# Kernel optimization log

Hardware: AMD Instinct MI355X
Metric: run time of the kernel (lower is better)

The kernel has to match this reference:

```python
import jax, jax.numpy as jnp
import numpy as np

D_MODEL, D_FF, N_EXPERTS, TOP_K = 1024, 2048, 8, 2
B, S = 2, 2048

def setup_inputs() -> dict:
    key = jax.random.key(0)
    k1, k2, k3, k4 = jax.random.split(key, 4)
    scale = 0.02
    return {
        "x": jax.random.normal(k1, (B, S, D_MODEL), dtype=jnp.float32),
        "gate_w": jax.random.normal(k2, (D_MODEL, N_EXPERTS), dtype=jnp.float32) * scale,
        "w1": jax.random.normal(k3, (N_EXPERTS, D_MODEL, D_FF), dtype=jnp.float32) * scale,
        "w2": jax.random.normal(k4, (N_EXPERTS, D_FF, D_MODEL), dtype=jnp.float32) * scale,
    }

def reference(x, gate_w, w1, w2):
    # --- Router (eval mode: no exploration noise, no dropout) ---
    router_logits = jnp.einsum('bsd,de->bse', x, gate_w)          # [B,S,E]
    top_logits, top_idx = jax.lax.top_k(router_logits, TOP_K)      # [B,S,K]
    top_w = jax.nn.softmax(top_logits, axis=-1)                    # [B,S,K]
    # topk indices are distinct per token, so per-(token,expert) combine weight
    # is the sum over k of weight_k * 1[idx_k == e] (matches torch gather/argmax logic)
    combine = jnp.sum(
        jax.nn.one_hot(top_idx, N_EXPERTS, dtype=x.dtype) * top_w[..., None],
        axis=-2)                                                   # [B,S,E]
    # --- Experts: dense-compute formulation of the gather/MLP/scatter loop ---
    h = jax.nn.silu(jnp.einsum('bsd,edf->ebsf', x, w1))            # [E,B,S,Dff]
    y = jnp.einsum('ebsf,efd->ebsd', h, w2)                        # [E,B,S,D]
    out = jnp.einsum('ebsd,bse->bsd', y, combine)                  # [B,S,D]
    return out
```

## Files before the change

### kernel.cpp

```cpp
#include <hip/hip_runtime.h>
#include <cstdint>
#include <cstddef>

#define D_MODEL 1024
#define D_FF    2048
#define N_EXP   8
#define NTOK    4096
#define NASSIGN (NTOK * 2)
#define MAXTILE 72

typedef __bf16 bf16_t;
typedef bf16_t bf16x8 __attribute__((ext_vector_type(8)));
typedef float  f32x4  __attribute__((ext_vector_type(4)));

typedef __attribute__((address_space(3))) void       lds_void;
typedef const __attribute__((address_space(1))) void gl_void;

__device__ __forceinline__ unsigned short f2b(float f) {
  union { float f; unsigned u; } v; v.f = f;
  unsigned u = v.u;
  unsigned r = (u + 0x7FFFu + ((u >> 16) & 1u)) >> 16;
  return (unsigned short)r;
}
__device__ __forceinline__ float b2f(unsigned short b) {
  union { unsigned u; float f; } v; v.u = ((unsigned)b) << 16; return v.f;
}

__device__ __forceinline__ void transpose_tile(
    const float* __restrict__ ein, unsigned short* __restrict__ eout,
    int R, int C, int bx, int by, float (*T)[65], int tid)
{
  const int c0 = bx * 64, r0 = by * 64;
  const int g = tid >> 4;
  const int m = tid & 15;
  #pragma unroll
  for (int i = 0; i < 4; ++i) {
    int r = i * 16 + g;
    float4 v = *(const float4*)(ein + (size_t)(r0 + r) * C + c0 + m * 4);
    T[r][m * 4 + 0] = v.x; T[r][m * 4 + 1] = v.y;
    T[r][m * 4 + 2] = v.z; T[r][m * 4 + 3] = v.w;
  }
  __syncthreads();
  #pragma unroll
  for (int i = 0; i < 4; ++i) {
    int c = i * 16 + g;
    ushort4 o;
    o.x = f2b(T[m * 4 + 0][c]); o.y = f2b(T[m * 4 + 1][c]);
    o.z = f2b(T[m * 4 + 2][c]); o.w = f2b(T[m * 4 + 3][c]);
    *(ushort4*)(eout + (size_t)(c0 + c) * R + r0 + m * 4) = o;
  }
}

__global__ __launch_bounds__(256) void prep_k(
    const float* __restrict__ x, const float* __restrict__ gw,
    const float* __restrict__ w1, const float* __restrict__ w2,
    unsigned short* __restrict__ w1t, unsigned short* __restrict__ w2t,
    int* __restrict__ eidx, float* __restrict__ ewt)
{
  __shared__ float T[64][65];
  const int bid = blockIdx.x;
  const int tid = threadIdx.x;

  if (bid < 4096) {
    int bx = bid & 31, by = (bid >> 5) & 15, e = bid >> 9;
    transpose_tile(w1 + (size_t)e * D_MODEL * D_FF,
                   w1t + (size_t)e * D_MODEL * D_FF,
                   D_MODEL, D_FF, bx, by, T, tid);
    return;
  }
  if (bid < 8192) {
    int b = bid - 4096;
    int bx = b & 15, by = (b >> 4) & 31, e = b >> 9;
    transpose_tile(w2 + (size_t)e * D_MODEL * D_FF,
                   w2t + (size_t)e * D_MODEL * D_FF,
                   D_FF, D_MODEL, bx, by, T, tid);
    return;
  }
  const int rb = bid - 8192;
  const int wv = tid >> 6, lane = tid & 63;
  const int token = rb * 4 + wv;
  const float4* xr4 = (const float4*)(x + (size_t)token * D_MODEL);
  const float4* gw4 = (const float4*)gw;

  float acc[8] = {};
  #pragma unroll
  for (int it = 0; it < 4; ++it) {
    float4 xv = xr4[it * 64 + lane];
    int d0 = it * 256 + lane * 4;
    #pragma unroll
    for (int i = 0; i < 4; ++i) {
      int d = d0 + i;
      float4 g0 = gw4[d * 2];
      float4 g1 = gw4[d * 2 + 1];
      float xs = (i == 0) ? xv.x : (i == 1) ? xv.y : (i == 2) ? xv.z : xv.w;
      acc[0] += xs * g0.x; acc[1] += xs * g0.y;
      acc[2] += xs * g0.z; acc[3] += xs * g0.w;
      acc[4] += xs * g1.x; acc[5] += xs * g1.y;
      acc[6] += xs * g1.z; acc[7] += xs * g1.w;
    }
  }
  #pragma unroll
  for (int m = 1; m < 64; m <<= 1) {
    #pragma unroll
    for (int k = 0; k < 8; ++k) acc[k] += __shfl_xor(acc[k], m);
  }
  if (lane == 0) {
    int i1 = 0; float v1 = acc[0];
    #pragma unroll
    for (int k = 1; k < 8; ++k) if (acc[k] > v1) { v1 = acc[k]; i1 = k; }
    int i2 = -1; float v2 = -1e30f;
    #pragma unroll
    for (int k = 0; k < 8; ++k) if (k != i1 && acc[k] > v2) { v2 = acc[k]; i2 = k; }
    float t  = __expf(v2 - v1);
    float wa = 1.f / (1.f + t);
    float wb = t * wa;
    eidx[token * 2 + 0] = i1; eidx[token * 2 + 1] = i2;
    ewt [token * 2 + 0] = wa; ewt [token * 2 + 1] = wb;
  }
}

__global__ __launch_bounds__(256) void scan_k(
    const int* __restrict__ eidx, const float* __restrict__ ewt,
    int* __restrict__ counts, int* __restrict__ offsets,
    int* __restrict__ rowtok, float* __restrict__ rowwt, int* __restrict__ rowof,
    int* __restrict__ tile_e, int* __restrict__ tile_m0, int* __restrict__ tile_n)
{
  __shared__ int hist[256][9];
  __shared__ int soff[8];
  const int t = threadIdx.x;

  int local[8] = {};
  #pragma unroll 4
  for (int i = 0; i < 32; ++i) local[eidx[t * 32 + i]]++;
  #pragma unroll
  for (int e = 0; e < 8; ++e) hist[t][e] = local[e];
  __syncthreads();

  for (int ofs = 1; ofs < 256; ofs <<= 1) {
    int v[8];
    if (t >= ofs) {
      #pragma unroll
      for (int e = 0; e < 8; ++e) v[e] = hist[t - ofs][e];
    }
    __syncthreads();
    if (t >= ofs) {
      #pragma unroll
      for (int e = 0; e < 8; ++e) hist[t][e] += v[e];
    }
    __syncthreads();
  }

  if (t == 0) {
    int o = 0, tt = 0;
    for (int e = 0; e < 8; ++e) {
      int c = hist[255][e];
      counts[e] = c;
      offsets[e] = o;
      soff[e] = o;
      int nt = (c + 127) >> 7;
      for (int i = 0; i < nt; ++i) { tile_e[tt] = e; tile_m0[tt] = i * 128; ++tt; }
      o += c;
    }
    tile_n[0] = tt;
  }
  __syncthreads();

  int run[8];
  #pragma unroll
  for (int e = 0; e < 8; ++e) run[e] = soff[e] + hist[t][e] - local[e];

  #pragma unroll 4
  for (int i = 0; i < 32; ++i) {
    int b = t * 32 + i;
    int e = eidx[b];
    int row = run[e]++;
    rowtok[row] = b >> 1;
    rowwt[row]  = ewt[b];
    rowof[b]    = row;
  }
}

__global__ __launch_bounds__(256) void gather_k(
    const float* __restrict__ x, const int* __restrict__ rowtok,
    unsigned short* __restrict__ Xe)
{
  const int row = blockIdx.x;
  const int token = rowtok[row];
  const float4* xr = (const float4*)(x + (size_t)token * D_MODEL);
  ushort4* dst = (ushort4*)(Xe + (size_t)row * D_MODEL);
  float4 v = xr[threadIdx.x];
  ushort4 o;
  o.x = f2b(v.x); o.y = f2b(v.y); o.z = f2b(v.z); o.w = f2b(v.w);
  dst[threadIdx.x] = o;
}

template<int K, int N, int NT_LOG2, int MODE>
__global__ __launch_bounds__(256) void moe_gemm_k(
    const unsigned short* __restrict__ A,
    const unsigned short* __restrict__ Bt,
    unsigned short* __restrict__ Hout,
    const int* __restrict__ counts, const int* __restrict__ offsets,
    const float* __restrict__ rowwt,
    const int* __restrict__ tile_e, const int* __restrict__ tile_m0,
    const int* __restrict__ tile_n)
{
  const int t = blockIdx.x >> NT_LOG2;
  if (t >= tile_n[0]) return;
  const int e   = tile_e[t];
  const int m0  = tile_m0[t];
  const int n0  = (blockIdx.x & ((1 << NT_LOG2) - 1)) * 128;
  const int cnt = counts[e];
  const int base = offsets[e];

  __shared__ unsigned short lA[128 * 32];
  __shared__ unsigned short lB[128 * 32];

  const int tid = threadIdx.x;
  const int lane = tid & 63;
  const int wv = tid >> 6;
  const int wm = wv & 1, wn = wv >> 1;
  const int col = lane & 15, quad = lane >> 4;

  const unsigned short* Aseg = A + (size_t)base * K;
  const unsigned short* Bseg = Bt + (size_t)e * ((size_t)N * K);

  const int lrow = lane >> 2;
  const int gch  = (lane & 3) ^ ((lane >> 2) & 3) ^ ((lane >> 4) & 3);

  const int fsw = (col & 3) ^ ((col >> 2) & 3);

  f32x4 acc[4][4] = {};

  for (int k0 = 0; k0 < K; k0 += 32) {
    __syncthreads();
    #pragma unroll
    for (int r = 0; r < 2; ++r) {
      int s = r * 4 + wv;
      int row = s * 16 + lrow;
      const char* gA = (const char*)Aseg + ((size_t)(m0 + row) * K + k0) * 2 + gch * 16;
      const char* gB = (const char*)Bseg + ((size_t)(n0 + row) * K + k0) * 2 + gch * 16;
      __builtin_amdgcn_global_load_lds((gl_void*)gA, (lds_void*)((char*)lA + s * 1024), 16, 0, 0);
      __builtin_amdgcn_global_load_lds((gl_void*)gB, (lds_void*)((char*)lB + s * 1024), 16, 0, 0);
    }
    __syncthreads();

    bf16x8 af[4], bfr[4];
    #pragma unroll
    for (int i = 0; i < 4; ++i) {
      int r = wm * 64 + i * 16 + col;
      int p = quad ^ fsw;
      af[i] = *(const bf16x8*)(lA + r * 32 + p * 8);
    }
    #pragma unroll
    for (int j = 0; j < 4; ++j) {
      int r = wn * 64 + j * 16 + col;
      int p = quad ^ fsw;
      bfr[j] = *(const bf16x8*)(lB + r * 32 + p * 8);
    }
    #pragma unroll
    for (int i = 0; i < 4; ++i)
      #pragma unroll
      for (int j = 0; j < 4; ++j)
        acc[i][j] = __builtin_amdgcn_mfma_f32_16x16x32_bf16(af[i], bfr[j], acc[i][j], 0, 0, 0);
  }

  #pragma unroll
  for (int i = 0; i < 4; ++i) {
    #pragma unroll
    for (int reg = 0; reg < 4; ++reg) {
      int r = m0 + wm * 64 + i * 16 + quad * 4 + reg;
      if (r < cnt) {
        unsigned short* hrow = Hout + (size_t)(base + r) * N + (n0 + wn * 64 + col);
        if (MODE == 1) {
          #pragma unroll
          for (int j = 0; j < 4; ++j) {
            float v = acc[i][j][reg];
            float s = v / (1.f + __expf(-v));
            hrow[j * 16] = f2b(s);
          }
        } else {
          float wgt = rowwt[base + r];
          #pragma unroll
          for (int j = 0; j < 4; ++j)
            hrow[j * 16] = f2b(wgt * acc[i][j][reg]);
        }
      }
    }
  }
}

__global__ __launch_bounds__(256) void combine_k(
    const unsigned short* __restrict__ Y, const int* __restrict__ rowof,
    float* __restrict__ out)
{
  const int token = blockIdx.x;
  const int r1 = rowof[token * 2];
  const int r2 = rowof[token * 2 + 1];
  const int d4 = threadIdx.x;
  ushort4 a = *(const ushort4*)(Y + (size_t)r1 * D_MODEL + d4 * 4);
  ushort4 b = *(const ushort4*)(Y + (size_t)r2 * D_MODEL + d4 * 4);
  float4 o;
  o.x = b2f(a.x) + b2f(b.x);
  o.y = b2f(a.y) + b2f(b.y);
  o.z = b2f(a.z) + b2f(b.z);
  o.w = b2f(a.w) + b2f(b.w);
  *(float4*)(out + (size_t)token * D_MODEL + d4 * 4) = o;
}

extern "C" void kernel_launch(void* const* d_in, const int* in_sizes, int n_in,
                              void* d_out, int out_size, void* d_ws, size_t ws_size,
                              hipStream_t stream) {
  const float* x  = (const float*)d_in[0];
  const float* gw = (const float*)d_in[1];
  const float* w1 = (const float*)d_in[2];
  const float* w2 = (const float*)d_in[3];
  float* out = (float*)d_out;

  char* ws = (char*)d_ws;
  size_t off = 0;
  auto alloc = [&](size_t bytes) -> char* {
    char* p = ws + off; off += (bytes + 255) & ~(size_t)255; return p;
  };
  int*   ctrl    = (int*)alloc(1024);
  int*   counts  = ctrl;
  int*   offsets = ctrl + 8;
  int*   tile_n  = ctrl + 16;
  int*   tile_e  = ctrl + 32;
  int*   tile_m0 = ctrl + 32 + MAXTILE;
  int*   eidx    = (int*)  alloc((size_t)NASSIGN * 4);
  float* ewt     = (float*)alloc((size_t)NASSIGN * 4);
  int*   rowtok  = (int*)  alloc((size_t)NASSIGN * 4);
  float* rowwt   = (float*)alloc((size_t)NASSIGN * 4);
  int*   rowof   = (int*)  alloc((size_t)NASSIGN * 4);
  unsigned short* Xe  = (unsigned short*)alloc((size_t)(NASSIGN + 128) * D_MODEL * 2);
  unsigned short* H   = (unsigned short*)alloc((size_t)(NASSIGN + 128) * D_FF * 2);
  unsigned short* Y   = (unsigned short*)alloc((size_t)(NASSIGN + 128) * D_MODEL * 2);
  unsigned short* w1t = (unsigned short*)alloc((size_t)N_EXP * D_MODEL * D_FF * 2);
  unsigned short* w2t = (unsigned short*)alloc((size_t)N_EXP * D_MODEL * D_FF * 2);

  prep_k<<<8192 + NTOK / 4, 256, 0, stream>>>(x, gw, w1, w2, w1t, w2t, eidx, ewt);
  scan_k<<<1, 256, 0, stream>>>(eidx, ewt, counts, offsets, rowtok, rowwt, rowof,
                                tile_e, tile_m0, tile_n);
  gather_k<<<NASSIGN, 256, 0, stream>>>(x, rowtok, Xe);

  moe_gemm_k<D_MODEL, D_FF, 4, 1><<<MAXTILE * 16, 256, 0, stream>>>(
      Xe, w1t, H, counts, offsets, rowwt, tile_e, tile_m0, tile_n);
  moe_gemm_k<D_FF, D_MODEL, 3, 2><<<MAXTILE * 8, 256, 0, stream>>>(
      H, w2t, Y, counts, offsets, rowwt, tile_e, tile_m0, tile_n);
  combine_k<<<NTOK, 256, 0, stream>>>(Y, rowof, out);
}
```

Before: 355.3 us.

## Transpose weight tile pairs via packed bf16 LDS, warp-shuffle scan, gemm occupancy hint

The weight transpose now does two 64x64 tiles per block. It converts to bf16 before staging, packs pairs into 32-bit LDS words, and issues all global loads up front, halving the block count and LDS traffic. The single-block scan uses 1024 threads with wave-level shuffle prefix sums in place of a shared-memory Hillis-Steele scan with many barriers. The expert GEMMs also gain a min-blocks launch-bounds hint, which may force register spilling.

```diff
diff --git a/kernel.cpp b/kernel.cpp
--- a/kernel.cpp
+++ b/kernel.cpp
@@ -26,28 +26,56 @@
   union { unsigned u; float f; } v; v.u = ((unsigned)b) << 16; return v.f;
 }
 
-__device__ __forceinline__ void transpose_tile(
+__device__ __forceinline__ void transpose_pair(
     const float* __restrict__ ein, unsigned short* __restrict__ eout,
-    int R, int C, int bx, int by, float (*T)[65], int tid)
-{
-  const int c0 = bx * 64, r0 = by * 64;
+    int R, int C, int c00, int r0, unsigned* T0, unsigned* T1, int tid)
+{
   const int g = tid >> 4;
   const int m = tid & 15;
-  #pragma unroll
-  for (int i = 0; i < 4; ++i) {
-    int r = i * 16 + g;
-    float4 v = *(const float4*)(ein + (size_t)(r0 + r) * C + c0 + m * 4);
-    T[r][m * 4 + 0] = v.x; T[r][m * 4 + 1] = v.y;
-    T[r][m * 4 + 2] = v.z; T[r][m * 4 + 3] = v.w;
-  }
-  __syncthreads();
+  const int sh = (g & 1) * 16;
+
+  float4 v[2][4];
+  #pragma unroll
+  for (int t = 0; t < 2; ++t)
+    #pragma unroll
+    for (int i = 0; i < 4; ++i)
+      v[t][i] = *(const float4*)(ein + (size_t)(r0 + i * 16 + g) * C + (c00 + t * 64) + m * 4);
+
+  #pragma unroll
+  for (int i = 0; i < 4; ++i) {
+    unsigned lo = (unsigned)f2b(v[0][i].x) | ((unsigned)f2b(v[0][i].y) << 16);
+    unsigned hi = (unsigned)f2b(v[0][i].z) | ((unsigned)f2b(v[0][i].w) << 16);
+    unsigned* p = T0 + (i * 16 + g) * 33 + m * 2;
+    p[0] = lo; p[1] = hi;
+  }
+  __syncthreads();
+  #pragma unroll
+  for (int i = 0; i < 4; ++i) {
+    unsigned lo = (unsigned)f2b(v[1][i].x) | ((unsigned)f2b(v[1][i].y) << 16);
+    unsigned hi = (unsigned)f2b(v[1][i].z) | ((unsigned)f2b(v[1][i].w) << 16);
+    unsigned* p = T1 + (i * 16 + g) * 33 + m * 2;
+    p[0] = lo; p[1] = hi;
+  }
   #pragma unroll
   for (int i = 0; i < 4; ++i) {
     int c = i * 16 + g;
     ushort4 o;
-    o.x = f2b(T[m * 4 + 0][c]); o.y = f2b(T[m * 4 + 1][c]);
-    o.z = f2b(T[m * 4 + 2][c]); o.w = f2b(T[m * 4 + 3][c]);
-    *(ushort4*)(eout + (size_t)(c0 + c) * R + r0 + m * 4) = o;
+    o.x = (unsigned short)(T0[(4 * m + 0) * 33 + (c >> 1)] >> sh);
+    o.y = (unsigned short)(T0[(4 * m + 1) * 33 + (c >> 1)] >> sh);
+    o.z = (unsigned short)(T0[(4 * m + 2) * 33 + (c >> 1)] >> sh);
+    o.w = (unsigned short)(T0[(4 * m + 3) * 33 + (c >> 1)] >> sh);
+    *(ushort4*)(eout + (size_t)(c00 + c) * R + r0 + m * 4) = o;
+  }
+  __syncthreads();
+  #pragma unroll
+  for (int i = 0; i < 4; ++i) {
+    int c = i * 16 + g;
+    ushort4 o;
+    o.x = (unsigned short)(T1[(4 * m + 0) * 33 + (c >> 1)] >> sh);
+    o.y = (unsigned short)(T1[(4 * m + 1) * 33 + (c >> 1)] >> sh);
+    o.z = (unsigned short)(T1[(4 * m + 2) * 33 + (c >> 1)] >> sh);
+    o.w = (unsigned short)(T1[(4 * m + 3) * 33 + (c >> 1)] >> sh);
+    *(ushort4*)(eout + (size_t)(c00 + c + 64) * R + r0 + m * 4) = o;
   }
 }
 
@@ -57,26 +85,28 @@
     unsigned short* __restrict__ w1t, unsigned short* __restrict__ w2t,
     int* __restrict__ eidx, float* __restrict__ ewt)
 {
-  __shared__ float T[64][65];
+  __shared__ unsigned T[2][64 * 33];
   const int bid = blockIdx.x;
   const int tid = threadIdx.x;
 
+  if (bid < 2048) {
+    int e = bid >> 8, rem = bid & 255;
+    int bx2 = rem & 15, by = rem >> 4;
+    transpose_pair(w1 + (size_t)e * D_MODEL * D_FF,
+                   w1t + (size_t)e * D_MODEL * D_FF,
+                   D_MODEL, D_FF, bx2 * 128, by * 64, T[0], T[1], tid);
+    return;
+  }
   if (bid < 4096) {
-    int bx = bid & 31, by = (bid >> 5) & 15, e = bid >> 9;
-    transpose_tile(w1 + (size_t)e * D_MODEL * D_FF,
-                   w1t + (size_t)e * D_MODEL * D_FF,
-                   D_MODEL, D_FF, bx, by, T, tid);
+    int b = bid - 2048;
+    int e = b >> 8, rem = b & 255;
+    int bx2 = rem & 7, by = rem >> 3;
+    transpose_pair(w2 + (size_t)e * D_MODEL * D_FF,
+                   w2t + (size_t)e * D_MODEL * D_FF,
+                   D_FF, D_MODEL, bx2 * 128, by * 64, T[0], T[1], tid);
     return;
   }
-  if (bid < 8192) {
-    int b = bid - 4096;
-    int bx = b & 15, by = (b >> 4) & 31, e = b >> 9;
-    transpose_tile(w2 + (size_t)e * D_MODEL * D_FF,
-                   w2t + (size_t)e * D_MODEL * D_FF,
-                   D_FF, D_MODEL, bx, by, T, tid);
-    return;
-  }
-  const int rb = bid - 8192;
+  const int rb = bid - 4096;
   const int wv = tid >> 6, lane = tid & 63;
   const int token = rb * 4 + wv;
   const float4* xr4 = (const float4*)(x + (size_t)token * D_MODEL);
@@ -119,41 +149,53 @@
   }
 }
 
-__global__ __launch_bounds__(256) void scan_k(
+__global__ __launch_bounds__(1024) void scan_k(
     const int* __restrict__ eidx, const float* __restrict__ ewt,
     int* __restrict__ counts, int* __restrict__ offsets,
     int* __restrict__ rowtok, float* __restrict__ rowwt, int* __restrict__ rowof,
     int* __restrict__ tile_e, int* __restrict__ tile_m0, int* __restrict__ tile_n)
 {
-  __shared__ int hist[256][9];
+  __shared__ int wtot[16][9];
+  __shared__ int woff[16][9];
   __shared__ int soff[8];
-  const int t = threadIdx.x;
-
-  int local[8] = {};
-  #pragma unroll 4
-  for (int i = 0; i < 32; ++i) local[eidx[t * 32 + i]]++;
-  #pragma unroll
-  for (int e = 0; e < 8; ++e) hist[t][e] = local[e];
-  __syncthreads();
-
-  for (int ofs = 1; ofs < 256; ofs <<= 1) {
-    int v[8];
-    if (t >= ofs) {
-      #pragma unroll
-      for (int e = 0; e < 8; ++e) v[e] = hist[t - ofs][e];
-    }
-    __syncthreads();
-    if (t >= ofs) {
-      #pragma unroll
-      for (int e = 0; e < 8; ++e) hist[t][e] += v[e];
-    }
-    __syncthreads();
-  }
+  const int t = threadIdx.x, w = t >> 6, lane = t & 63;
+
+  int4 a = ((const int4*)eidx)[t * 2];
+  int4 b = ((const int4*)eidx)[t * 2 + 1];
+  int my[8] = {a.x, a.y, a.z, a.w, b.x, b.y, b.z, b.w};
+  int pre[8], local[8] = {};
+  #pragma unroll
+  for (int i = 0; i < 8; ++i) { pre[i] = local[my[i]]; local[my[i]]++; }
+
+  int inc[8];
+  #pragma unroll
+  for (int e = 0; e < 8; ++e) inc[e] = local[e];
+  #pragma unroll
+  for (int d = 1; d < 64; d <<= 1) {
+    #pragma unroll
+    for (int e = 0; e < 8; ++e) {
+      int v = __shfl_up(inc[e], d);
+      if (lane >= d) inc[e] += v;
+    }
+  }
+  if (lane == 63) {
+    #pragma unroll
+    for (int e = 0; e < 8; ++e) wtot[w][e] = inc[e];
+  }
+  __syncthreads();
+
+  if (t < 8) {
+    int e = t, run = 0;
+    #pragma unroll
+    for (int ww = 0; ww < 16; ++ww) { woff[ww][e] = run; run += wtot[ww][e]; }
+    wtot[0][e] = run;
+  }
+  __syncthreads();
 
   if (t == 0) {
     int o = 0, tt = 0;
     for (int e = 0; e < 8; ++e) {
-      int c = hist[255][e];
+      int c = wtot[0][e];
       counts[e] = c;
       offsets[e] = o;
       soff[e] = o;
@@ -165,18 +207,21 @@
   }
   __syncthreads();
 
-  int run[8];
-  #pragma unroll
-  for (int e = 0; e < 8; ++e) run[e] = soff[e] + hist[t][e] - local[e];
-
-  #pragma unroll 4
-  for (int i = 0; i < 32; ++i) {
-    int b = t * 32 + i;
-    int e = eidx[b];
-    int row = run[e]++;
-    rowtok[row] = b >> 1;
-    rowwt[row]  = ewt[b];
-    rowof[b]    = row;
+  int base_[8];
+  #pragma unroll
+  for (int e = 0; e < 8; ++e) base_[e] = soff[e] + woff[w][e] + inc[e] - local[e];
+
+  float4 wa4 = ((const float4*)ewt)[t * 2];
+  float4 wb4 = ((const float4*)ewt)[t * 2 + 1];
+  float wv[8] = {wa4.x, wa4.y, wa4.z, wa4.w, wb4.x, wb4.y, wb4.z, wb4.w};
+
+  #pragma unroll
+  for (int i = 0; i < 8; ++i) {
+    int bb = t * 8 + i, e = my[i];
+    int row = base_[e] + pre[i];
+    rowtok[row] = bb >> 1;
+    rowwt[row]  = wv[i];
+    rowof[bb]   = row;
   }
 }
 
@@ -195,7 +240,7 @@
 }
 
 template<int K, int N, int NT_LOG2, int MODE>
-__global__ __launch_bounds__(256) void moe_gemm_k(
+__global__ __launch_bounds__(256, 6) void moe_gemm_k(
     const unsigned short* __restrict__ A,
     const unsigned short* __restrict__ Bt,
     unsigned short* __restrict__ Hout,
@@ -226,8 +271,7 @@
 
   const int lrow = lane >> 2;
   const int gch  = (lane & 3) ^ ((lane >> 2) & 3) ^ ((lane >> 4) & 3);
-
-  const int fsw = (col & 3) ^ ((col >> 2) & 3);
+  const int fsw  = (col & 3) ^ ((col >> 2) & 3);
 
   f32x4 acc[4][4] = {};
 
@@ -338,9 +382,9 @@
   unsigned short* w1t = (unsigned short*)alloc((size_t)N_EXP * D_MODEL * D_FF * 2);
   unsigned short* w2t = (unsigned short*)alloc((size_t)N_EXP * D_MODEL * D_FF * 2);
 
-  prep_k<<<8192 + NTOK / 4, 256, 0, stream>>>(x, gw, w1, w2, w1t, w2t, eidx, ewt);
-  scan_k<<<1, 256, 0, stream>>>(eidx, ewt, counts, offsets, rowtok, rowwt, rowof,
-                                tile_e, tile_m0, tile_n);
+  prep_k<<<4096 + NTOK / 4, 256, 0, stream>>>(x, gw, w1, w2, w1t, w2t, eidx, ewt);
+  scan_k<<<1, 1024, 0, stream>>>(eidx, ewt, counts, offsets, rowtok, rowwt, rowof,
+                                 tile_e, tile_m0, tile_n);
   gather_k<<<NASSIGN, 256, 0, stream>>>(x, rowtok, Xe);
 
   moe_gemm_k<D_MODEL, D_FF, 4, 1><<<MAXTILE * 16, 256, 0, stream>>>(
```

Result: slower. 918.4 us (+158.5%).
